# Kernel tuning notes

Measured on AMD Instinct MI355X. Metric: run time of the kernel, lower is better.

The kernel has to match this reference:

```python
import jax, jax.numpy as jnp
import numpy as np

EPS = 1e-3  # keras LayerNormalization default epsilon

def layer_norm(x, gamma, beta):
    mu = jnp.mean(x, axis=-1, keepdims=True)
    var = jnp.var(x, axis=-1, keepdims=True)
    return (x - mu) * jax.lax.rsqrt(var + EPS) * gamma + beta

def setup_inputs() -> dict:
    key = jax.random.key(0)
    ks = jax.random.split(key, 10)
    B, N, FD, AD, PD, DP = 4, 512, 256, 256, 128, 64
    s = lambda k, *sh: jax.random.normal(k, sh, dtype=jnp.float32)
    return {
        "F": s(ks[0], B, N, FD),
        "D": s(ks[1], B, N, N, DP),
        "Wq": s(ks[2], FD, AD) / np.sqrt(FD),
        "Wk": s(ks[3], FD, AD) / np.sqrt(FD),
        "Wv": s(ks[4], FD, AD) / np.sqrt(FD),
        "g_f": jnp.ones((FD,), jnp.float32),
        "b_f": jnp.zeros((FD,), jnp.float32),
        "g_p": jnp.ones((DP,), jnp.float32),
        "b_p": jnp.zeros((DP,), jnp.float32),
        "W_pt": s(ks[5], DP, PD) / np.sqrt(DP),
        "b_pt": jnp.zeros((PD,), jnp.float32),
        "W_ph": s(ks[6], PD, 1) / np.sqrt(PD),
    }

def reference(F, D, Wq, Wk, Wv, g_f, b_f, g_p, b_p, W_pt, b_pt, W_ph):
    # features path
    Fn = layer_norm(F, g_f, b_f)                       # [B,N,FD]
    Q = Fn @ Wq                                        # [B,N,AD]
    K = Fn @ Wk
    V = Fn @ Wv
    # pair-bias path: LN -> Dense(pairs_dim)+bias -> Dense(num_heads=1)
    Bn = layer_norm(D, g_p, b_p)                       # [B,N,N,DP]
    Bt = Bn @ W_pt + b_pt                              # [B,N,N,PD]
    bias = (Bt @ W_ph)[..., 0]                         # [B,N,N]
    scalar = 1.0 / jnp.sqrt(jnp.float32(Q.shape[-1]))
    A = jnp.einsum('bqd,bkd->bqk', Q, K) + bias        # QK^T + pair bias
    A = jax.nn.softmax(scalar * A, axis=-1)
    O = jnp.einsum('bqk,bkd->bqd', A, V)               # [B,N,AD]
    return jnp.sum(O, axis=-1)                         # [B,N]
```

## Files before the change

### kernel.cpp

```cpp
#include <hip/hip_runtime.h>
#include <hip/hip_bf16.h>
#include <cstddef>

#define OFF_GW    0
#define OFF_SC    320
#define OFF_VSUM  384
#define OFF_Q     2432
#define OFF_K     526720

typedef float v4f __attribute__((ext_vector_type(4)));

__global__ __launch_bounds__(256) void k1_fused(
    const float* __restrict__ F, const float* __restrict__ Wq,
    const float* __restrict__ Wk, const float* __restrict__ Wv,
    const float* __restrict__ g_f, const float* __restrict__ b_f,
    const float* __restrict__ g_p, const float* __restrict__ b_p,
    const float* __restrict__ W_pt, const float* __restrict__ b_pt,
    const float* __restrict__ W_ph, float* __restrict__ ws) {
  int t = threadIdx.x;
  int bid = blockIdx.x;

  if (bid < 512) {
    __shared__ __align__(16) float fn[8][260];
    __shared__ float smu[8], srn[8];
    int g = bid >> 1, h = bid & 1;
    int row0 = g * 8;
    const float* Fp = F + (size_t)row0 * 256;
#pragma unroll
    for (int k = 0; k < 8; ++k) fn[k][t] = Fp[k * 256 + t];
    __syncthreads();
    int r = t >> 5, l32 = t & 31;
    float s1 = 0.f, s2 = 0.f;
#pragma unroll
    for (int m = 0; m < 8; ++m) {
      float x = fn[r][l32 + 32 * m];
      s1 += x;
      s2 += x * x;
    }
    for (int m = 16; m >= 1; m >>= 1) {
      s1 += __shfl_xor(s1, m);
      s2 += __shfl_xor(s2, m);
    }
    if (l32 == 0) {
      float mu = s1 * (1.f / 256.f);
      float var = s2 * (1.f / 256.f) - mu * mu;
      smu[r] = mu;
      srn[r] = rsqrtf(var + 1e-3f);
    }
    __syncthreads();
    float gf = g_f[t], bf = b_f[t];
#pragma unroll
    for (int k = 0; k < 8; ++k)
      fn[k][t] = (fn[k][t] - smu[k]) * srn[k] * gf + bf;
    __syncthreads();
    int matsel = t >> 7;
    int col = h * 128 + (t & 127);
    const float* W = matsel ? Wk : Wq;
    float acc[8] = {0, 0, 0, 0, 0, 0, 0, 0};
#pragma unroll 2
    for (int f = 0; f < 256; f += 4) {
      float w0 = W[(f + 0) * 256 + col];
      float w1 = W[(f + 1) * 256 + col];
      float w2 = W[(f + 2) * 256 + col];
      float w3 = W[(f + 3) * 256 + col];
#pragma unroll
      for (int k = 0; k < 8; ++k) {
        v4f x = *(const v4f*)(&fn[k][f]);
        acc[k] = fmaf(x.w, w3,
                 fmaf(x.z, w2, fmaf(x.y, w1, fmaf(x.x, w0, acc[k]))));
      }
    }
    float* Out = ws + (matsel ? OFF_K : OFF_Q) + (size_t)row0 * 256 + col;
#pragma unroll
    for (int k = 0; k < 8; ++k) Out[k * 256] = acc[k];

  } else if (bid < 576) {
    __shared__ float wv_s[256];
    __shared__ float u_s[256];
    __shared__ float sc_s[2];
    int vb = bid - 512;
    int w = t >> 6, l = t & 63;
    for (int rr = 0; rr < 64; ++rr) {
      int row = 64 * w + rr;
      float s = 0.f;
#pragma unroll
      for (int j = 0; j < 4; ++j) s += Wv[row * 256 + l + 64 * j];
      for (int m = 32; m >= 1; m >>= 1) s += __shfl_xor(s, m);
      if (l == 0) wv_s[row] = s;
    }
    __syncthreads();
    u_s[t] = g_f[t] * wv_s[t];
    __syncthreads();
    if (w == 0) {
      float a1 = u_s[l] + u_s[l + 64] + u_s[l + 128] + u_s[l + 192];
      float a2 = b_f[l] * wv_s[l] + b_f[l + 64] * wv_s[l + 64] +
                 b_f[l + 128] * wv_s[l + 128] + b_f[l + 192] * wv_s[l + 192];
      for (int m = 32; m >= 1; m >>= 1) {
        a1 += __shfl_xor(a1, m);
        a2 += __shfl_xor(a2, m);
      }
      if (l == 0) {
        sc_s[0] = a1;
        sc_s[1] = a2;
      }
    }
    __syncthreads();
    float sgu = sc_s[0], sbv = sc_s[1];
    for (int rr = 0; rr < 8; ++rr) {
      int row = vb * 32 + w * 8 + rr;
      float s1 = 0.f, s2 = 0.f, sw = 0.f;
#pragma unroll
      for (int j = 0; j < 4; ++j) {
        float x = F[(size_t)row * 256 + l + 64 * j];
        s1 += x;
        s2 += x * x;
        sw += x * u_s[l + 64 * j];
      }
      for (int m = 32; m >= 1; m >>= 1) {
        s1 += __shfl_xor(s1, m);
        s2 += __shfl_xor(s2, m);
        sw += __shfl_xor(sw, m);
      }
      if (l == 0) {
        float mu = s1 * (1.f / 256.f);
        float var = s2 * (1.f / 256.f) - mu * mu;
        float rn = rsqrtf(var + 1e-3f);
        ws[OFF_VSUM + row] = rn * (sw - mu * sgu) + sbv;
      }
    }

  } else {
    __shared__ float wc_s[64];
    __shared__ float wph_s[128];
    if (t < 128) wph_s[t] = W_ph[t];
    __syncthreads();
    int c = t >> 2, sub = t & 3;
    float wc = 0.f;
#pragma unroll
    for (int j = 0; j < 32; ++j)
      wc += W_pt[c * 128 + sub * 32 + j] * wph_s[sub * 32 + j];
    wc += __shfl_xor(wc, 1);
    wc += __shfl_xor(wc, 2);
    if (sub == 0) {
      wc_s[c] = wc;
      ws[OFF_GW + c] = g_p[c] * wc;
    }
    __syncthreads();
    if (t == 0) {
      float sg = 0.f, bc = 0.f;
      for (int cc = 0; cc < 64; ++cc) {
        sg += g_p[cc] * wc_s[cc];
        bc += b_p[cc] * wc_s[cc];
      }
      for (int p = 0; p < 128; ++p) bc += b_pt[p] * wph_s[p];
      ws[OFF_SC] = sg;
      ws[OFF_SC + 1] = bc;
    }
  }
}

__global__ __launch_bounds__(256) void kb_bias_attn(
    const float* __restrict__ D, const float* __restrict__ ws,
    float* __restrict__ out) {
  __shared__ float4 Qs4[4][64];
  __shared__ float Sx[4][512];
  __shared__ float vs[512];
  int t = threadIdx.x;
  int b = blockIdx.x >> 7;
  int tile = blockIdx.x & 127;
  int q0 = tile * 4;
  int rowbase = b * 512 + q0;
  float* qsf = (float*)Qs4;
#pragma unroll
  for (int k = 0; k < 4; ++k)
    qsf[k * 256 + t] = ws[OFF_Q + (size_t)(rowbase + k) * 256 + t];
  vs[t] = ws[OFF_VSUM + b * 512 + t];
  vs[t + 256] = ws[OFF_VSUM + b * 512 + 256 + t];
  float sum_gw = ws[OFF_SC];
  float bconst = ws[OFF_SC + 1];
  int qq = t & 3;
  float4 g[4];
#pragma unroll
  for (int j = 0; j < 4; ++j) g[j] = ((const float4*)(ws + OFF_GW))[qq * 4 + j];

  int e4 = t >> 2;
  const float* Dbase = D + (size_t)rowbase * 512 * 64;
#pragma unroll 4
  for (int pi = 0; pi < 32; ++pi) {
    int rr = pi >> 3;
    int kk = (pi & 7) * 64 + e4;
    const v4f* dp =
        (const v4f*)(Dbase + ((size_t)rr * 512 + kk) * 64 + qq * 16);
    float s1 = 0.f, s2 = 0.f, sw = 0.f;
#pragma unroll
    for (int j = 0; j < 4; ++j) {
      v4f x = __builtin_nontemporal_load(dp + j);
      s1 += x.x + x.y + x.z + x.w;
      s2 += x.x * x.x + x.y * x.y + x.z * x.z + x.w * x.w;
      sw += x.x * g[j].x + x.y * g[j].y + x.z * g[j].z + x.w * g[j].w;
    }
    s1 += __shfl_xor(s1, 1);
    s2 += __shfl_xor(s2, 1);
    sw += __shfl_xor(sw, 1);
    s1 += __shfl_xor(s1, 2);
    s2 += __shfl_xor(s2, 2);
    sw += __shfl_xor(sw, 2);
    if (qq == 0) {
      float mu = s1 * (1.f / 64.f);
      float var = s2 * (1.f / 64.f) - mu * mu;
      float rn = rsqrtf(var + 1e-3f);
      Sx[rr][kk] = (rn * (sw - mu * sum_gw) + bconst) * 0.0625f;
    }
  }
  __syncthreads();

  const float* Kg = ws + OFF_K;
  const float4* K0p = (const float4*)(Kg + (size_t)(b * 512 + t) * 256);
  const float4* K1p = (const float4*)(Kg + (size_t)(b * 512 + 256 + t) * 256);
  float a0[4] = {0, 0, 0, 0}, a1[4] = {0, 0, 0, 0};
#pragma unroll 4
  for (int f = 0; f < 64; ++f) {
    float4 kv0 = K0p[f];
    float4 kv1 = K1p[f];
#pragma unroll
    for (int rr = 0; rr < 4; ++rr) {
      float4 qv = Qs4[rr][f];
      a0[rr] += qv.x * kv0.x + qv.y * kv0.y + qv.z * kv0.z + qv.w * kv0.w;
      a1[rr] += qv.x * kv1.x + qv.y * kv1.y + qv.z * kv1.z + qv.w * kv1.w;
    }
  }
#pragma unroll
  for (int rr = 0; rr < 4; ++rr) {
    Sx[rr][t] += a0[rr] * 0.0625f;
    Sx[rr][t + 256] += a1[rr] * 0.0625f;
  }
  __syncthreads();

  int w = t >> 6, l = t & 63;
  float m = -1e30f;
#pragma unroll
  for (int j = 0; j < 8; ++j) m = fmaxf(m, Sx[w][l + 64 * j]);
  for (int mm = 32; mm >= 1; mm >>= 1) m = fmaxf(m, __shfl_xor(m, mm));
  float se = 0.f, sv = 0.f;
#pragma unroll
  for (int j = 0; j < 8; ++j) {
    float ev = __expf(Sx[w][l + 64 * j] - m);
    se += ev;
    sv += ev * vs[l + 64 * j];
  }
  for (int mm = 32; mm >= 1; mm >>= 1) {
    se += __shfl_xor(se, mm);
    sv += __shfl_xor(sv, mm);
  }
  if (l == 0) out[rowbase + w] = sv / se;
}

extern "C" void kernel_launch(void* const* d_in, const int* in_sizes, int n_in,
                              void* d_out, int out_size, void* d_ws,
                              size_t ws_size, hipStream_t stream) {
  const float* F    = (const float*)d_in[0];
  const float* D    = (const float*)d_in[1];
  const float* Wq   = (const float*)d_in[2];
  const float* Wk   = (const float*)d_in[3];
  const float* Wv   = (const float*)d_in[4];
  const float* g_f  = (const float*)d_in[5];
  const float* b_f  = (const float*)d_in[6];
  const float* g_p  = (const float*)d_in[7];
  const float* b_p  = (const float*)d_in[8];
  const float* W_pt = (const float*)d_in[9];
  const float* b_pt = (const float*)d_in[10];
  const float* W_ph = (const float*)d_in[11];
  float* out = (float*)d_out;
  float* ws = (float*)d_ws;

  k1_fused<<<577, 256, 0, stream>>>(F, Wq, Wk, Wv, g_f, b_f, g_p, b_p, W_pt,
                                    b_pt, W_ph, ws);
  kb_bias_attn<<<512, 256, 0, stream>>>(D, ws, out);
}
```

Before: 461.2 us.

## Fuse projection and bias-attention kernels with per-batch atomic counter barrier

```diff
diff --git a/kernel.cpp b/kernel.cpp
--- a/kernel.cpp
+++ b/kernel.cpp
@@ -2,138 +2,40 @@
 #include <hip/hip_bf16.h>
 #include <cstddef>
 
-#define OFF_GW    0
-#define OFF_SC    320
-#define OFF_VSUM  384
-#define OFF_Q     2432
-#define OFF_K     526720
+#define OFF_CTR   0
+#define OFF_VSUM  64
+#define OFF_K     4096
 
 typedef float v4f __attribute__((ext_vector_type(4)));
 
-__global__ __launch_bounds__(256) void k1_fused(
-    const float* __restrict__ F, const float* __restrict__ Wq,
-    const float* __restrict__ Wk, const float* __restrict__ Wv,
-    const float* __restrict__ g_f, const float* __restrict__ b_f,
-    const float* __restrict__ g_p, const float* __restrict__ b_p,
-    const float* __restrict__ W_pt, const float* __restrict__ b_pt,
-    const float* __restrict__ W_ph, float* __restrict__ ws) {
+__global__ __launch_bounds__(256) void fused_all(
+    const float* __restrict__ F, const float* __restrict__ D,
+    const float* __restrict__ Wq, const float* __restrict__ Wk,
+    const float* __restrict__ Wv, const float* __restrict__ g_f,
+    const float* __restrict__ b_f, const float* __restrict__ g_p,
+    const float* __restrict__ b_p, const float* __restrict__ W_pt,
+    const float* __restrict__ b_pt, const float* __restrict__ W_ph,
+    float* __restrict__ ws, float* __restrict__ out) {
+  __shared__ float wph_s[128];
+  __shared__ float wc_s[64];
+  __shared__ __align__(16) float gw_s[64];
+  __shared__ float sc_s[2];
+  __shared__ float smu[4], srn[4];
+  __shared__ __align__(16) float fn[4][260];
+  __shared__ float wv_s[256];
+  __shared__ __align__(16) float Qs[4][256];
+  __shared__ float Sx[4][512];
+  __shared__ float vs[512];
+
   int t = threadIdx.x;
-  int bid = blockIdx.x;
-
-  if (bid < 512) {
-    __shared__ __align__(16) float fn[8][260];
-    __shared__ float smu[8], srn[8];
-    int g = bid >> 1, h = bid & 1;
-    int row0 = g * 8;
-    const float* Fp = F + (size_t)row0 * 256;
-#pragma unroll
-    for (int k = 0; k < 8; ++k) fn[k][t] = Fp[k * 256 + t];
-    __syncthreads();
-    int r = t >> 5, l32 = t & 31;
-    float s1 = 0.f, s2 = 0.f;
-#pragma unroll
-    for (int m = 0; m < 8; ++m) {
-      float x = fn[r][l32 + 32 * m];
-      s1 += x;
-      s2 += x * x;
-    }
-    for (int m = 16; m >= 1; m >>= 1) {
-      s1 += __shfl_xor(s1, m);
-      s2 += __shfl_xor(s2, m);
-    }
-    if (l32 == 0) {
-      float mu = s1 * (1.f / 256.f);
-      float var = s2 * (1.f / 256.f) - mu * mu;
-      smu[r] = mu;
-      srn[r] = rsqrtf(var + 1e-3f);
-    }
-    __syncthreads();
-    float gf = g_f[t], bf = b_f[t];
-#pragma unroll
-    for (int k = 0; k < 8; ++k)
-      fn[k][t] = (fn[k][t] - smu[k]) * srn[k] * gf + bf;
-    __syncthreads();
-    int matsel = t >> 7;
-    int col = h * 128 + (t & 127);
-    const float* W = matsel ? Wk : Wq;
-    float acc[8] = {0, 0, 0, 0, 0, 0, 0, 0};
-#pragma unroll 2
-    for (int f = 0; f < 256; f += 4) {
-      float w0 = W[(f + 0) * 256 + col];
-      float w1 = W[(f + 1) * 256 + col];
-      float w2 = W[(f + 2) * 256 + col];
-      float w3 = W[(f + 3) * 256 + col];
-#pragma unroll
-      for (int k = 0; k < 8; ++k) {
-        v4f x = *(const v4f*)(&fn[k][f]);
-        acc[k] = fmaf(x.w, w3,
-                 fmaf(x.z, w2, fmaf(x.y, w1, fmaf(x.x, w0, acc[k]))));
-      }
-    }
-    float* Out = ws + (matsel ? OFF_K : OFF_Q) + (size_t)row0 * 256 + col;
-#pragma unroll
-    for (int k = 0; k < 8; ++k) Out[k * 256] = acc[k];
-
-  } else if (bid < 576) {
-    __shared__ float wv_s[256];
-    __shared__ float u_s[256];
-    __shared__ float sc_s[2];
-    int vb = bid - 512;
-    int w = t >> 6, l = t & 63;
-    for (int rr = 0; rr < 64; ++rr) {
-      int row = 64 * w + rr;
-      float s = 0.f;
-#pragma unroll
-      for (int j = 0; j < 4; ++j) s += Wv[row * 256 + l + 64 * j];
-      for (int m = 32; m >= 1; m >>= 1) s += __shfl_xor(s, m);
-      if (l == 0) wv_s[row] = s;
-    }
-    __syncthreads();
-    u_s[t] = g_f[t] * wv_s[t];
-    __syncthreads();
-    if (w == 0) {
-      float a1 = u_s[l] + u_s[l + 64] + u_s[l + 128] + u_s[l + 192];
-      float a2 = b_f[l] * wv_s[l] + b_f[l + 64] * wv_s[l + 64] +
-                 b_f[l + 128] * wv_s[l + 128] + b_f[l + 192] * wv_s[l + 192];
-      for (int m = 32; m >= 1; m >>= 1) {
-        a1 += __shfl_xor(a1, m);
-        a2 += __shfl_xor(a2, m);
-      }
-      if (l == 0) {
-        sc_s[0] = a1;
-        sc_s[1] = a2;
-      }
-    }
-    __syncthreads();
-    float sgu = sc_s[0], sbv = sc_s[1];
-    for (int rr = 0; rr < 8; ++rr) {
-      int row = vb * 32 + w * 8 + rr;
-      float s1 = 0.f, s2 = 0.f, sw = 0.f;
-#pragma unroll
-      for (int j = 0; j < 4; ++j) {
-        float x = F[(size_t)row * 256 + l + 64 * j];
-        s1 += x;
-        s2 += x * x;
-        sw += x * u_s[l + 64 * j];
-      }
-      for (int m = 32; m >= 1; m >>= 1) {
-        s1 += __shfl_xor(s1, m);
-        s2 += __shfl_xor(s2, m);
-        sw += __shfl_xor(sw, m);
-      }
-      if (l == 0) {
-        float mu = s1 * (1.f / 256.f);
-        float var = s2 * (1.f / 256.f) - mu * mu;
-        float rn = rsqrtf(var + 1e-3f);
-        ws[OFF_VSUM + row] = rn * (sw - mu * sgu) + sbv;
-      }
-    }
-
-  } else {
-    __shared__ float wc_s[64];
-    __shared__ float wph_s[128];
-    if (t < 128) wph_s[t] = W_ph[t];
-    __syncthreads();
+  int b = blockIdx.x >> 7;
+  int tile = blockIdx.x & 127;
+  int rowbase = b * 512 + tile * 4;
+  int w = t >> 6, l = t & 63;
+
+  if (t < 128) wph_s[t] = W_ph[t];
+  __syncthreads();
+  {
     int c = t >> 2, sub = t & 3;
     float wc = 0.f;
 #pragma unroll
@@ -143,46 +45,101 @@
     wc += __shfl_xor(wc, 2);
     if (sub == 0) {
       wc_s[c] = wc;
-      ws[OFF_GW + c] = g_p[c] * wc;
-    }
-    __syncthreads();
-    if (t == 0) {
-      float sg = 0.f, bc = 0.f;
-      for (int cc = 0; cc < 64; ++cc) {
-        sg += g_p[cc] * wc_s[cc];
-        bc += b_p[cc] * wc_s[cc];
+      gw_s[c] = g_p[c] * wc;
+    }
+  }
+  __syncthreads();
+  if (w == 0) {
+    float a1 = g_p[l] * wc_s[l];
+    float a2 = b_p[l] * wc_s[l] + b_pt[l] * wph_s[l] +
+               b_pt[l + 64] * wph_s[l + 64];
+    for (int m = 32; m >= 1; m >>= 1) {
+      a1 += __shfl_xor(a1, m);
+      a2 += __shfl_xor(a2, m);
+    }
+    if (l == 0) {
+      sc_s[0] = a1;
+      sc_s[1] = a2;
+    }
+  }
+  for (int rr = 0; rr < 64; ++rr) {
+    int row = 64 * w + rr;
+    float s = 0.f;
+#pragma unroll
+    for (int j = 0; j < 4; ++j) s += Wv[row * 256 + l + 64 * j];
+    for (int m = 32; m >= 1; m >>= 1) s += __shfl_xor(s, m);
+    if (l == 0) wv_s[row] = s;
+  }
+#pragma unroll
+  for (int k = 0; k < 4; ++k) fn[k][t] = F[(size_t)(rowbase + k) * 256 + t];
+  __syncthreads();
+  {
+    float s1 = 0.f, s2 = 0.f;
+#pragma unroll
+    for (int m = 0; m < 4; ++m) {
+      float x = fn[w][l + 64 * m];
+      s1 += x;
+      s2 += x * x;
+    }
+    for (int m = 32; m >= 1; m >>= 1) {
+      s1 += __shfl_xor(s1, m);
+      s2 += __shfl_xor(s2, m);
+    }
+    if (l == 0) {
+      float mu = s1 * (1.f / 256.f);
+      float var = s2 * (1.f / 256.f) - mu * mu;
+      smu[w] = mu;
+      srn[w] = rsqrtf(var + 1e-3f);
+    }
+  }
+  __syncthreads();
+  {
+    float gf = g_f[t], bf = b_f[t];
+#pragma unroll
+    for (int k = 0; k < 4; ++k)
+      fn[k][t] = (fn[k][t] - smu[k]) * srn[k] * gf + bf;
+  }
+  __syncthreads();
+  {
+    float s = 0.f;
+#pragma unroll
+    for (int m = 0; m < 4; ++m) s += fn[w][l + 64 * m] * wv_s[l + 64 * m];
+    for (int m = 32; m >= 1; m >>= 1) s += __shfl_xor(s, m);
+    if (l == 0) ws[OFF_VSUM + rowbase + w] = s;
+  }
+  {
+    float qa[4] = {0, 0, 0, 0}, ka[4] = {0, 0, 0, 0};
+#pragma unroll 2
+    for (int f = 0; f < 256; f += 4) {
+      float wq0 = Wq[(f + 0) * 256 + t], wq1 = Wq[(f + 1) * 256 + t];
+      float wq2 = Wq[(f + 2) * 256 + t], wq3 = Wq[(f + 3) * 256 + t];
+      float wk0 = Wk[(f + 0) * 256 + t], wk1 = Wk[(f + 1) * 256 + t];
+      float wk2 = Wk[(f + 2) * 256 + t], wk3 = Wk[(f + 3) * 256 + t];
+#pragma unroll
+      for (int k = 0; k < 4; ++k) {
+        v4f x = *(const v4f*)(&fn[k][f]);
+        qa[k] = fmaf(x.x, wq0,
+                fmaf(x.y, wq1, fmaf(x.z, wq2, fmaf(x.w, wq3, qa[k]))));
+        ka[k] = fmaf(x.x, wk0,
+                fmaf(x.y, wk1, fmaf(x.z, wk2, fmaf(x.w, wk3, ka[k]))));
       }
-      for (int p = 0; p < 128; ++p) bc += b_pt[p] * wph_s[p];
-      ws[OFF_SC] = sg;
-      ws[OFF_SC + 1] = bc;
-    }
-  }
-}
-
-__global__ __launch_bounds__(256) void kb_bias_attn(
-    const float* __restrict__ D, const float* __restrict__ ws,
-    float* __restrict__ out) {
-  __shared__ float4 Qs4[4][64];
-  __shared__ float Sx[4][512];
-  __shared__ float vs[512];
-  int t = threadIdx.x;
-  int b = blockIdx.x >> 7;
-  int tile = blockIdx.x & 127;
-  int q0 = tile * 4;
-  int rowbase = b * 512 + q0;
-  float* qsf = (float*)Qs4;
-#pragma unroll
-  for (int k = 0; k < 4; ++k)
-    qsf[k * 256 + t] = ws[OFF_Q + (size_t)(rowbase + k) * 256 + t];
-  vs[t] = ws[OFF_VSUM + b * 512 + t];
-  vs[t + 256] = ws[OFF_VSUM + b * 512 + 256 + t];
-  float sum_gw = ws[OFF_SC];
-  float bconst = ws[OFF_SC + 1];
+    }
+#pragma unroll
+    for (int k = 0; k < 4; ++k) {
+      Qs[k][t] = qa[k];
+      ws[OFF_K + (size_t)(rowbase + k) * 256 + t] = ka[k];
+    }
+  }
+  __threadfence();
+  __syncthreads();
+  if (t == 0) atomicAdd((int*)ws + b, 1);
+
+  float sum_gw = sc_s[0];
+  float bconst = sc_s[1];
   int qq = t & 3;
-  float4 g[4];
-#pragma unroll
-  for (int j = 0; j < 4; ++j) g[j] = ((const float4*)(ws + OFF_GW))[qq * 4 + j];
-
+  v4f g[4];
+#pragma unroll
+  for (int j = 0; j < 4; ++j) g[j] = *(const v4f*)(&gw_s[qq * 16 + j * 4]);
   int e4 = t >> 2;
   const float* Dbase = D + (size_t)rowbase * 512 * 64;
 #pragma unroll 4
@@ -212,19 +169,29 @@
       Sx[rr][kk] = (rn * (sw - mu * sum_gw) + bconst) * 0.0625f;
     }
   }
-  __syncthreads();
+
+  if (t == 0) {
+    while (__hip_atomic_load((int*)ws + b, __ATOMIC_ACQUIRE,
+                             __HIP_MEMORY_SCOPE_AGENT) < 128) {
+      __builtin_amdgcn_s_sleep(8);
+    }
+  }
+  __syncthreads();
+
+  vs[t] = ws[OFF_VSUM + b * 512 + t];
+  vs[t + 256] = ws[OFF_VSUM + b * 512 + 256 + t];
 
   const float* Kg = ws + OFF_K;
-  const float4* K0p = (const float4*)(Kg + (size_t)(b * 512 + t) * 256);
-  const float4* K1p = (const float4*)(Kg + (size_t)(b * 512 + 256 + t) * 256);
+  const v4f* K0p = (const v4f*)(Kg + (size_t)(b * 512 + t) * 256);
+  const v4f* K1p = (const v4f*)(Kg + (size_t)(b * 512 + 256 + t) * 256);
   float a0[4] = {0, 0, 0, 0}, a1[4] = {0, 0, 0, 0};
 #pragma unroll 4
   for (int f = 0; f < 64; ++f) {
-    float4 kv0 = K0p[f];
-    float4 kv1 = K1p[f];
+    v4f kv0 = K0p[f];
+    v4f kv1 = K1p[f];
 #pragma unroll
     for (int rr = 0; rr < 4; ++rr) {
-      float4 qv = Qs4[rr][f];
+      v4f qv = *(const v4f*)(&Qs[rr][f * 4]);
       a0[rr] += qv.x * kv0.x + qv.y * kv0.y + qv.z * kv0.z + qv.w * kv0.w;
       a1[rr] += qv.x * kv1.x + qv.y * kv1.y + qv.z * kv1.z + qv.w * kv1.w;
     }
@@ -236,7 +203,6 @@
   }
   __syncthreads();
 
-  int w = t >> 6, l = t & 63;
   float m = -1e30f;
 #pragma unroll
   for (int j = 0; j < 8; ++j) m = fmaxf(m, Sx[w][l + 64 * j]);
@@ -273,7 +239,7 @@
   float* out = (float*)d_out;
   float* ws = (float*)d_ws;
 
-  k1_fused<<<577, 256, 0, stream>>>(F, Wq, Wk, Wv, g_f, b_f, g_p, b_p, W_pt,
-                                    b_pt, W_ph, ws);
-  kb_bias_attn<<<512, 256, 0, stream>>>(D, ws, out);
+  hipMemsetAsync(d_ws, 0, 16, stream);
+  fused_all<<<512, 256, 0, stream>>>(F, D, Wq, Wk, Wv, g_f, b_f, g_p, b_p,
+                                     W_pt, b_pt, W_ph, ws, out);
 }
```

After: 530.2 us. 1.15x slower.
